# Optimization experiments

Measured on AMD Instinct MI355X. Metric: run time of the kernel, lower is better.

## Reference

```python
import jax, jax.numpy as jnp
import numpy as np

N = 100000   # nodes
E = 3200000  # edges (avg degree 32)
D = 128      # embed_dim
H = 512      # FF hidden
EPS = 1e-5   # BatchNorm eps


def setup_inputs() -> dict:
    key = jax.random.key(0)
    ks = jax.random.split(key, 10)
    x = jax.random.normal(ks[0], (N, D), dtype=jnp.float32)
    edge_index = jax.random.randint(ks[1], (2, E), 0, N, dtype=jnp.int32)
    s = 1.0 / np.sqrt(D)
    W = jax.random.uniform(ks[2], (D, D), jnp.float32, -s, s)   # GCNConv weight
    b = jnp.zeros((D,), jnp.float32)                             # GCNConv bias
    gamma = jnp.ones((D,), jnp.float32)                          # shared BN affine
    beta = jnp.zeros((D,), jnp.float32)
    s1 = 1.0 / np.sqrt(D)
    w1 = jax.random.uniform(ks[3], (D, H), jnp.float32, -s1, s1)
    b1 = jax.random.uniform(ks[4], (H,), jnp.float32, -s1, s1)
    s2 = 1.0 / np.sqrt(H)
    w2 = jax.random.uniform(ks[5], (H, D), jnp.float32, -s2, s2)
    b2 = jax.random.uniform(ks[6], (D,), jnp.float32, -s2, s2)
    return {"x": x, "edge_index": edge_index, "W": W, "b": b,
            "gamma": gamma, "beta": beta, "w1": w1, "b1": b1, "w2": w2, "b2": b2}


def batchnorm(x, gamma, beta):
    # training-mode BatchNorm1d over node dim, biased variance
    mu = jnp.mean(x, axis=0)
    var = jnp.mean(jnp.square(x - mu), axis=0)
    return (x - mu) * jax.lax.rsqrt(var + EPS) * gamma + beta


def gcn_conv(x, edge_index, W, b):
    # PyG GCNConv: add self-loops, sym-normalize, linear, scatter-add, bias
    n = x.shape[0]
    loops = jnp.arange(n, dtype=edge_index.dtype)
    src = jnp.concatenate([edge_index[0], loops])
    dst = jnp.concatenate([edge_index[1], loops])
    xw = x @ W                                                    # [N, D]
    deg = jax.ops.segment_sum(jnp.ones_like(dst, x.dtype), dst, num_segments=n)
    dinv = jax.lax.rsqrt(deg)                                     # deg >= 1 (self-loops)
    norm = dinv[src] * dinv[dst]                                  # [E+N]
    msg = xw[src] * norm[:, None]                                 # [E+N, D] gather
    out = jax.ops.segment_sum(msg, dst, num_segments=n)           # scatter-add
    return out + b


def reference(x, edge_index, W, b, gamma, beta, w1, b1, w2, b2):
    h = gcn_conv(x, edge_index, W, b)
    x = batchnorm(x + h, gamma, beta)
    ff = jax.nn.relu(x @ w1 + b1) @ w2 + b2
    return batchnorm(x + ff, gamma, beta)
```

## Files before the change

### kernel.cpp

```cpp
#include <hip/hip_runtime.h>
#include <hip/hip_bf16.h>
#include <stdint.h>

#define NN 100000
#define NE 3200000
#define DIM 128
#define HID 512
#define BN_EPS 1e-5f
#define NBIN 128
#define NPBIN 784
#define TILE 2048
#define CAP 27000

typedef short short8 __attribute__((ext_vector_type(8)));
typedef float floatx4 __attribute__((ext_vector_type(4)));

__device__ __forceinline__ float bfu2f(unsigned short u) {
    return __uint_as_float(((unsigned int)u) << 16);
}
__device__ __forceinline__ unsigned short f2bfu(float f) {
    union { __hip_bfloat16 h; unsigned short u; } cv;
    cv.h = __float2bfloat16(f);
    return cv.u;
}

__global__ void k_init(int* __restrict__ bincur, float* __restrict__ stats) {
    int i = blockIdx.x * 256 + threadIdx.x;
    if (i < NBIN) bincur[i] = i * CAP;
    if (i < 512) stats[i] = 0.f;
}

__global__ __launch_bounds__(256) void k_fill1(const int* __restrict__ src, const int* __restrict__ dst,
                                               int* __restrict__ bincur, unsigned int* __restrict__ recs) {
    __shared__ int lhist[NBIN], lbase[NBIN], gbase[NBIN];
    __shared__ unsigned int lrec[TILE];
    int tid = threadIdx.x;
    int tbase = blockIdx.x * TILE;
    if (tid < NBIN) lhist[tid] = 0;
    __syncthreads();
    unsigned int myrec[8];
    int mybin[8], myrank[8];
    #pragma unroll
    for (int j = 0; j < 8; ++j) {
        int e = tbase + j * 256 + tid;
        mybin[j] = -1;
        if (e < NE) {
            int d = __builtin_nontemporal_load(dst + e);
            int s = __builtin_nontemporal_load(src + e);
            int b = d / NPBIN;
            myrec[j] = (unsigned)s | ((unsigned)(d - b * NPBIN) << 17);
            mybin[j] = b;
            myrank[j] = atomicAdd(&lhist[b], 1);
        }
    }
    __syncthreads();
    if (tid == 0) {
        int run = 0;
        #pragma unroll
        for (int b = 0; b < NBIN; ++b) { lbase[b] = run; run += lhist[b]; }
    }
    __syncthreads();
    if (tid < NBIN) gbase[tid] = atomicAdd(&bincur[tid], lhist[tid]);
    __syncthreads();
    #pragma unroll
    for (int j = 0; j < 8; ++j)
        if (mybin[j] >= 0) lrec[lbase[mybin[j]] + myrank[j]] = myrec[j];
    __syncthreads();
    int total = lbase[NBIN - 1] + lhist[NBIN - 1];
    for (int i = tid; i < total; i += 256) {
        int b = 0;
        #pragma unroll
        for (int st = NBIN / 2; st > 0; st >>= 1)
            if (b + st < NBIN && lbase[b + st] <= i) b += st;
        int p = gbase[b] + (i - lbase[b]);
        if (p < (b + 1) * CAP) recs[p] = lrec[i];
    }
}

__global__ __launch_bounds__(256) void k_cnt(const unsigned int* __restrict__ recs,
                                             const int* __restrict__ bincur,
                                             int* __restrict__ cnt) {
    __shared__ int lhist[NPBIN];
    int b = blockIdx.x;
    int tid = threadIdx.x;
    for (int i = tid; i < NPBIN; i += 256) lhist[i] = 0;
    __syncthreads();
    int start = b * CAP;
    int end = bincur[b];
    if (end > start + CAP) end = start + CAP;
    if (end < start) end = start;
    for (int i = start + tid; i < end; i += 256) {
        unsigned int r = __builtin_nontemporal_load(recs + i);
        int dl = (int)(r >> 17);
        if (dl < NPBIN) atomicAdd(&lhist[dl], 1);
    }
    __syncthreads();
    for (int i = tid; i < NPBIN; i += 256) {
        int n = b * NPBIN + i;
        if (n < NN) cnt[n] = lhist[i];
    }
}

__global__ __launch_bounds__(1024) void k_scanA(const int* __restrict__ cnt, int* __restrict__ offs,
                                                int* __restrict__ bsum, float* __restrict__ dinv) {
    __shared__ int wsum[16];
    int t = threadIdx.x;
    int lane = t & 63, wid = t >> 6;
    int i = blockIdx.x * 1024 + t;
    int v = (i < NN) ? cnt[i] : 0;
    int incl = v;
    #pragma unroll
    for (int off = 1; off < 64; off <<= 1) {
        int y = __shfl_up(incl, off, 64);
        if (lane >= off) incl += y;
    }
    if (lane == 63) wsum[wid] = incl;
    __syncthreads();
    if (wid == 0) {
        int wv = (lane < 16) ? wsum[lane] : 0;
        int wincl = wv;
        #pragma unroll
        for (int off = 1; off < 16; off <<= 1) {
            int y = __shfl_up(wincl, off, 64);
            if (lane >= off) wincl += y;
        }
        if (lane < 16) wsum[lane] = wincl - wv;
    }
    __syncthreads();
    int excl = wsum[wid] + incl - v;
    if (i < NN) {
        offs[i] = excl;
        dinv[i] = rsqrtf((float)(v + 1));
    }
    if (t == 1023) bsum[blockIdx.x] = excl + v;
}

__global__ __launch_bounds__(128) void k_scanB(int* __restrict__ bsum, int* __restrict__ offs, int nblk) {
    int t = threadIdx.x;
    if (t < 64) {
        int v = (t < nblk) ? bsum[t] : 0;
        int v2 = (t + 64 < nblk) ? bsum[t + 64] : 0;
        int incl = v;
        #pragma unroll
        for (int off = 1; off < 64; off <<= 1) {
            int y = __shfl_up(incl, off, 64);
            if (t >= off) incl += y;
        }
        int tot0 = __shfl(incl, 63, 64);
        int incl2 = v2;
        #pragma unroll
        for (int off = 1; off < 64; off <<= 1) {
            int y = __shfl_up(incl2, off, 64);
            if (t >= off) incl2 += y;
        }
        if (t < nblk) bsum[t] = incl - v;
        if (t + 64 < nblk) bsum[t + 64] = tot0 + incl2 - v2;
        if (t == 63) offs[NN] = tot0 + __shfl(incl2, 63, 64);
    }
}

__global__ void k_scanC(int* __restrict__ offs, const int* __restrict__ bsum) {
    int i = blockIdx.x * 256 + threadIdx.x;
    if (i < NN) offs[i] += bsum[i >> 10];
}

__global__ __launch_bounds__(256) void k_fill2(const unsigned int* __restrict__ recs,
                                               const int* __restrict__ bincur,
                                               const int* __restrict__ offs,
                                               int* __restrict__ srcs) {
    __shared__ int loffs[NPBIN], lcur[NPBIN];
    int b = blockIdx.x;
    int tid = threadIdx.x;
    for (int i = tid; i < NPBIN; i += 256) {
        int n = b * NPBIN + i;
        loffs[i] = (n <= NN) ? offs[n] : NE;
        lcur[i] = 0;
    }
    __syncthreads();
    int start = b * CAP;
    int end = bincur[b];
    if (end > start + CAP) end = start + CAP;
    if (end < start) end = start;
    for (int i = start + tid; i < end; i += 256) {
        unsigned int r = __builtin_nontemporal_load(recs + i);
        int s = (int)(r & 0x1FFFFu);
        int dl = (int)(r >> 17);
        if (dl < NPBIN) {
            int p = loffs[dl] + atomicAdd(&lcur[dl], 1);
            if ((unsigned)p < NE) srcs[p] = s;
        }
    }
}

__global__ void k_wt(const float* __restrict__ W, unsigned short* __restrict__ wt) {
    int i = blockIdx.x * 256 + threadIdx.x;
    if (i < DIM * DIM) {
        int k = i >> 7, n = i & 127;
        wt[n * DIM + k] = f2bfu(W[k * DIM + n]);
    }
}

__global__ void k_prep(const float* __restrict__ w1, const float* __restrict__ w2,
                       unsigned short* __restrict__ w1t, unsigned short* __restrict__ w2t) {
    int i = blockIdx.x * 256 + threadIdx.x;
    if (i < HID * DIM) {
        int n1 = i >> 7, k1 = i & 127;
        w1t[i] = f2bfu(w1[k1 * HID + n1]);
        int n2 = i & 127, k2 = i >> 7;
        w2t[n2 * HID + k2] = f2bfu(w2[k2 * DIM + n2]);
    }
}

__global__ __launch_bounds__(256) void k_gemm1(const float* __restrict__ x,
                                               const unsigned short* __restrict__ wt,
                                               const float* __restrict__ dinv,
                                               unsigned short* __restrict__ xw) {
    int wave = threadIdx.x >> 6;
    int lane = threadIdx.x & 63;
    int row0 = blockIdx.x * 64 + wave * 16;
    int arow = row0 + (lane & 15);
    if (arow >= NN) arow = NN - 1;
    int kbase = (lane >> 4) * 8;
    const float* xr = x + (size_t)arow * DIM;
    short8 afrag[4];
    #pragma unroll
    for (int kt = 0; kt < 4; ++kt) {
        float4 f0 = *(const float4*)(xr + kt * 32 + kbase);
        float4 f1 = *(const float4*)(xr + kt * 32 + kbase + 4);
        short8 a;
        a[0] = (short)f2bfu(f0.x); a[1] = (short)f2bfu(f0.y);
        a[2] = (short)f2bfu(f0.z); a[3] = (short)f2bfu(f0.w);
        a[4] = (short)f2bfu(f1.x); a[5] = (short)f2bfu(f1.y);
        a[6] = (short)f2bfu(f1.z); a[7] = (short)f2bfu(f1.w);
        afrag[kt] = a;
    }
    int crow = row0 + (lane >> 4) * 4;
    float dv[4];
    #pragma unroll
    for (int i = 0; i < 4; ++i) {
        int r = crow + i;
        dv[i] = dinv[r < NN ? r : NN - 1];
    }
    #pragma unroll
    for (int ct = 0; ct < 8; ++ct) {
        int ncol = ct * 16 + (lane & 15);
        const short* wr = (const short*)wt + (size_t)ncol * DIM;
        floatx4 acc = {0.f, 0.f, 0.f, 0.f};
        #pragma unroll
        for (int kt = 0; kt < 4; ++kt) {
            short8 bfrag = *(const short8*)(wr + kt * 32 + kbase);
            acc = __builtin_amdgcn_mfma_f32_16x16x32_bf16(afrag[kt], bfrag, acc, 0, 0, 0);
        }
        #pragma unroll
        for (int i = 0; i < 4; ++i) {
            int r = crow + i;
            if (r < NN) xw[(size_t)r * DIM + ct * 16 + (lane & 15)] = f2bfu(acc[i] * dv[i]);
        }
    }
}

__global__ __launch_bounds__(256) void k_aggregate(const unsigned int* __restrict__ xw2,
                                                   const int* __restrict__ offs,
                                                   const int* __restrict__ srcs,
                                                   const float* __restrict__ dinv,
                                                   const float* __restrict__ x,
                                                   const float* __restrict__ bias,
                                                   unsigned int* __restrict__ u) {
    int node = blockIdx.x * 4 + (threadIdx.x >> 6);
    if (node >= NN) return;
    int lane = threadIdx.x & 63;
    int qt = lane >> 4;
    int ql = lane & 15;
    int beg = offs[node], end = offs[node + 1];
    beg = max(0, min(beg, NE));
    end = max(beg, min(end, NE));
    int ne = end - beg;
    float a[8];
    #pragma unroll
    for (int j = 0; j < 8; ++j) a[j] = 0.f;
    const uint4* xw16 = (const uint4*)xw2;
    for (int base = 0; base < ne; base += 64) {
        int rem = ne - base;
        if (rem > 64) rem = 64;
        int sidx = (lane < rem) ? srcs[beg + base + lane] : 0;
        #pragma unroll 4
        for (int i = 0; i < rem; i += 4) {
            int want = i + qt;
            int s = __builtin_amdgcn_ds_bpermute(want << 2, sidx);
            if (want < rem) {
                if ((unsigned)s >= NN) s = 0;
                uint4 pk = xw16[(size_t)s * 16 + ql];
                a[0] += __uint_as_float(pk.x << 16);
                a[1] += __uint_as_float(pk.x & 0xffff0000u);
                a[2] += __uint_as_float(pk.y << 16);
                a[3] += __uint_as_float(pk.y & 0xffff0000u);
                a[4] += __uint_as_float(pk.z << 16);
                a[5] += __uint_as_float(pk.z & 0xffff0000u);
                a[6] += __uint_as_float(pk.w << 16);
                a[7] += __uint_as_float(pk.w & 0xffff0000u);
            }
        }
    }
    #pragma unroll
    for (int j = 0; j < 8; ++j) {
        a[j] += __shfl_xor(a[j], 16, 64);
        a[j] += __shfl_xor(a[j], 32, 64);
    }
    if (qt == 0) {
        uint4 ps = xw16[(size_t)node * 16 + ql];
        float di = dinv[node];
        const float* xr = x + (size_t)node * DIM + ql * 8;
        float4 xv0 = *(const float4*)xr;
        float4 xv1 = *(const float4*)(xr + 4);
        float4 bv0 = *(const float4*)(bias + ql * 8);
        float4 bv1 = *(const float4*)(bias + ql * 8 + 4);
        float o0 = xv0.x + bv0.x + di * (a[0] + __uint_as_float(ps.x << 16));
        float o1 = xv0.y + bv0.y + di * (a[1] + __uint_as_float(ps.x & 0xffff0000u));
        float o2 = xv0.z + bv0.z + di * (a[2] + __uint_as_float(ps.y << 16));
        float o3 = xv0.w + bv0.w + di * (a[3] + __uint_as_float(ps.y & 0xffff0000u));
        float o4 = xv1.x + bv1.x + di * (a[4] + __uint_as_float(ps.z << 16));
        float o5 = xv1.y + bv1.y + di * (a[5] + __uint_as_float(ps.z & 0xffff0000u));
        float o6 = xv1.z + bv1.z + di * (a[6] + __uint_as_float(ps.w << 16));
        float o7 = xv1.w + bv1.w + di * (a[7] + __uint_as_float(ps.w & 0xffff0000u));
        uint4 pk;
        pk.x = ((unsigned int)f2bfu(o1) << 16) | (unsigned int)f2bfu(o0);
        pk.y = ((unsigned int)f2bfu(o3) << 16) | (unsigned int)f2bfu(o2);
        pk.z = ((unsigned int)f2bfu(o5) << 16) | (unsigned int)f2bfu(o4);
        pk.w = ((unsigned int)f2bfu(o7) << 16) | (unsigned int)f2bfu(o6);
        ((uint4*)u)[(size_t)node * 16 + ql] = pk;
    }
}

__global__ void k_stats(const unsigned int* __restrict__ u2, float* __restrict__ stats) {
    int t = threadIdx.x;
    int c = t & 63, g = t >> 6;
    float s0 = 0.f, q0 = 0.f, s1 = 0.f, q1 = 0.f;
    for (int r = blockIdx.x * 4 + g; r < NN; r += gridDim.x * 4) {
        unsigned int pv = u2[(size_t)r * 64 + c];
        float x0 = __uint_as_float(pv << 16);
        float x1 = __uint_as_float(pv & 0xffff0000u);
        s0 += x0; q0 += x0 * x0; s1 += x1; q1 += x1 * x1;
    }
    __shared__ float A[256], B[256], C[256], D2[256];
    A[t] = s0; B[t] = q0; C[t] = s1; D2[t] = q1;
    __syncthreads();
    if (t < 64) {
        float rs0 = A[t] + A[t + 64] + A[t + 128] + A[t + 192];
        float rq0 = B[t] + B[t + 64] + B[t + 128] + B[t + 192];
        float rs1 = C[t] + C[t + 64] + C[t + 128] + C[t + 192];
        float rq1 = D2[t] + D2[t + 64] + D2[t + 128] + D2[t + 192];
        atomicAdd(&stats[2 * c],           rs0);
        atomicAdd(&stats[2 * c + 1],       rs1);
        atomicAdd(&stats[DIM + 2 * c],     rq0);
        atomicAdd(&stats[DIM + 2 * c + 1], rq1);
    }
}

__global__ void k_stats2(const float2* __restrict__ v2, float* __restrict__ stats) {
    int t = threadIdx.x;
    int c = t & 63, g = t >> 6;
    float s0 = 0.f, q0 = 0.f, s1 = 0.f, q1 = 0.f;
    for (int r = blockIdx.x * 4 + g; r < NN; r += gridDim.x * 4) {
        float2 pv = v2[(size_t)r * 64 + c];
        s0 += pv.x; q0 += pv.x * pv.x; s1 += pv.y; q1 += pv.y * pv.y;
    }
    __shared__ float A[256], B[256], C[256], D2[256];
    A[t] = s0; B[t] = q0; C[t] = s1; D2[t] = q1;
    __syncthreads();
    if (t < 64) {
        float rs0 = A[t] + A[t + 64] + A[t + 128] + A[t + 192];
        float rq0 = B[t] + B[t + 64] + B[t + 128] + B[t + 192];
        float rs1 = C[t] + C[t + 64] + C[t + 128] + C[t + 192];
        float rq1 = D2[t] + D2[t + 64] + D2[t + 128] + D2[t + 192];
        atomicAdd(&stats[2 * c],           rs0);
        atomicAdd(&stats[2 * c + 1],       rs1);
        atomicAdd(&stats[DIM + 2 * c],     rq0);
        atomicAdd(&stats[DIM + 2 * c + 1], rq1);
    }
}

__global__ __launch_bounds__(512) void k_ffx(const unsigned int* __restrict__ u2,
                                             const float* __restrict__ stats1,
                                             const float* __restrict__ gamma,
                                             const float* __restrict__ beta,
                                             const unsigned short* __restrict__ w1t,
                                             const float* __restrict__ b1,
                                             const unsigned short* __restrict__ w2t,
                                             const float* __restrict__ b2,
                                             float* __restrict__ v) {
    __shared__ __align__(16) float sscale[DIM], sshift[DIM];
    __shared__ __align__(16) unsigned int sw1[64 * 64];
    __shared__ __align__(16) unsigned int sw2[128 * 32];
    __shared__ __align__(16) unsigned int hbufs[8][16 * 32];
    int tid = threadIdx.x;
    if (tid < DIM) {
        float mu  = stats1[tid] * (1.0f / NN);
        float var = stats1[DIM + tid] * (1.0f / NN) - mu * mu;
        float sc = rsqrtf(var + BN_EPS) * gamma[tid];
        sscale[tid] = sc;
        sshift[tid] = beta[tid] - mu * sc;
    }
    __syncthreads();
    int wave = tid >> 6, lane = tid & 63;
    int m = lane & 15, q = lane >> 4;
    int nb = blockIdx.x * 256 + wave * 32;
    unsigned int* hb = &hbufs[wave][0];
    const int xsw = (m & 7) * 4;

    short8 yfrag[2][4];
    #pragma unroll
    for (int s = 0; s < 2; ++s) {
        int ng = nb + s * 16 + m;
        if (ng >= NN) ng = NN - 1;
        const uint4* up = (const uint4*)(u2 + (size_t)ng * 64);
        #pragma unroll
        for (int kt = 0; kt < 4; ++kt) {
            uint4 pv = up[kt * 4 + q];
            int c0 = kt * 32 + q * 8;
            float4 sa = *(const float4*)&sscale[c0], sb = *(const float4*)&sscale[c0 + 4];
            float4 ha = *(const float4*)&sshift[c0], hbv = *(const float4*)&sshift[c0 + 4];
            float f0 = __uint_as_float(pv.x << 16)         * sa.x + ha.x;
            float f1 = __uint_as_float(pv.x & 0xffff0000u) * sa.y + ha.y;
            float f2 = __uint_as_float(pv.y << 16)         * sa.z + ha.z;
            float f3 = __uint_as_float(pv.y & 0xffff0000u) * sa.w + ha.w;
            float f4 = __uint_as_float(pv.z << 16)         * sb.x + hbv.x;
            float f5 = __uint_as_float(pv.z & 0xffff0000u) * sb.y + hbv.y;
            float f6 = __uint_as_float(pv.w << 16)         * sb.z + hbv.z;
            float f7 = __uint_as_float(pv.w & 0xffff0000u) * sb.w + hbv.w;
            union { unsigned int u[4]; short8 sv; } yf;
            yf.u[0] = ((unsigned int)f2bfu(f1) << 16) | f2bfu(f0);
            yf.u[1] = ((unsigned int)f2bfu(f3) << 16) | f2bfu(f2);
            yf.u[2] = ((unsigned int)f2bfu(f5) << 16) | f2bfu(f4);
            yf.u[3] = ((unsigned int)f2bfu(f7) << 16) | f2bfu(f6);
            yfrag[s][kt] = yf.sv;
        }
    }

    floatx4 acc2[2][8];
    #pragma unroll
    for (int s = 0; s < 2; ++s)
        #pragma unroll
        for (int t = 0; t < 8; ++t) acc2[s][t] = (floatx4){0.f, 0.f, 0.f, 0.f};

    const uint4* w1g = (const uint4*)w1t;
    const uint4* w2g = (const uint4*)w2t;

    for (int c = 0; c < 8; ++c) {
        __syncthreads();
        #pragma unroll
        for (int it = 0; it < 2; ++it) {
            int i = tid + it * 512;
            int j = i >> 4, s4 = i & 15;
            uint4 val = w1g[(size_t)(c * 64 + j) * 16 + s4];
            *(uint4*)&sw1[j * 64 + ((s4 * 4) ^ ((j & 7) * 4))] = val;
        }
        #pragma unroll
        for (int it = 0; it < 2; ++it) {
            int i = tid + it * 512;
            int n = i >> 3, s4 = i & 7;
            uint4 val = w2g[(size_t)n * 64 + c * 8 + s4];
            *(uint4*)&sw2[n * 32 + ((s4 * 4) ^ ((n & 7) * 4))] = val;
        }
        __syncthreads();
        #pragma unroll
        for (int s = 0; s < 2; ++s) {
            floatx4 acc1[4];
            #pragma unroll
            for (int t = 0; t < 4; ++t) acc1[t] = (floatx4){0.f, 0.f, 0.f, 0.f};
            #pragma unroll
            for (int kt = 0; kt < 4; ++kt) {
                #pragma unroll
                for (int t = 0; t < 4; ++t) {
                    short8 wf = *(const short8*)&sw1[(t * 16 + m) * 64 + ((kt * 16 + q * 4) ^ xsw)];
                    acc1[t] = __builtin_amdgcn_mfma_f32_16x16x32_bf16(wf, yfrag[s][kt], acc1[t], 0, 0, 0);
                }
            }
            #pragma unroll
            for (int t = 0; t < 4; ++t) {
                float4 bb = *(const float4*)&b1[c * 64 + t * 16 + q * 4];
                float h0 = fmaxf(acc1[t][0] + bb.x, 0.f);
                float h1 = fmaxf(acc1[t][1] + bb.y, 0.f);
                float h2 = fmaxf(acc1[t][2] + bb.z, 0.f);
                float h3 = fmaxf(acc1[t][3] + bb.w, 0.f);
                uint2 hp;
                hp.x = ((unsigned int)f2bfu(h1) << 16) | f2bfu(h0);
                hp.y = ((unsigned int)f2bfu(h3) << 16) | f2bfu(h2);
                *(uint2*)&hb[m * 32 + ((t * 8 + q * 2) ^ xsw)] = hp;
            }
            #pragma unroll
            for (int kt = 0; kt < 2; ++kt) {
                short8 hf = *(const short8*)&hb[m * 32 + ((kt * 16 + q * 4) ^ xsw)];
                #pragma unroll
                for (int t = 0; t < 8; ++t) {
                    short8 wf2 = *(const short8*)&sw2[(t * 16 + m) * 32 + ((kt * 16 + q * 4) ^ xsw)];
                    acc2[s][t] = __builtin_amdgcn_mfma_f32_16x16x32_bf16(hf, wf2, acc2[s][t], 0, 0, 0);
                }
            }
        }
    }
    #pragma unroll
    for (int s = 0; s < 2; ++s) {
        #pragma unroll
        for (int t = 0; t < 8; ++t) {
            int col = t * 16 + m;
            float b2v = b2[col];
            float scl = sscale[col], shf = sshift[col];
            #pragma unroll
            for (int i = 0; i < 4; ++i) {
                int ng = nb + s * 16 + q * 4 + i;
                if (ng < NN) {
                    unsigned int pv = u2[(size_t)ng * 64 + (col >> 1)];
                    float uval = (col & 1) ? __uint_as_float(pv & 0xffff0000u)
                                           : __uint_as_float(pv << 16);
                    v[(size_t)ng * DIM + col] = acc2[s][t][i] + b2v + (uval * scl + shf);
                }
            }
        }
    }
}

__global__ void k_final(float* buf, const float* __restrict__ stats2,
                        const float* __restrict__ gamma,
                        const float* __restrict__ beta) {
    __shared__ float ssc[DIM], ssh[DIM];
    int t = threadIdx.x;
    if (t < DIM) {
        float mu  = stats2[t] * (1.0f / NN);
        float var = stats2[DIM + t] * (1.0f / NN) - mu * mu;
        float rsg = rsqrtf(var + BN_EPS) * gamma[t];
        ssc[t] = rsg;
        ssh[t] = beta[t] - mu * rsg;
    }
    __syncthreads();
    const int total = NN * DIM / 4;
    float4* b4 = (float4*)buf;
    for (int i = blockIdx.x * blockDim.x + t; i < total; i += gridDim.x * blockDim.x) {
        float4 val = b4[i];
        int c = (i * 4) & (DIM - 1);
        val.x = val.x * ssc[c]     + ssh[c];
        val.y = val.y * ssc[c + 1] + ssh[c + 1];
        val.z = val.z * ssc[c + 2] + ssh[c + 2];
        val.w = val.w * ssc[c + 3] + ssh[c + 3];
        b4[i] = val;
    }
}

extern "C" void kernel_launch(void* const* d_in, const int* in_sizes, int n_in,
                              void* d_out, int out_size, void* d_ws, size_t ws_size,
                              hipStream_t stream) {
    const float* x     = (const float*)d_in[0];
    const int*   ei    = (const int*)d_in[1];
    const float* W     = (const float*)d_in[2];
    const float* b     = (const float*)d_in[3];
    const float* gamma = (const float*)d_in[4];
    const float* beta  = (const float*)d_in[5];
    const float* w1    = (const float*)d_in[6];
    const float* b1    = (const float*)d_in[7];
    const float* w2    = (const float*)d_in[8];
    const float* b2    = (const float*)d_in[9];

    char* p = (char*)d_ws;
    auto alloc = [&](size_t bytes) { char* r = p; p += (bytes + 255) & ~(size_t)255; return r; };
    unsigned int*   u     = (unsigned int*)alloc((size_t)NN * DIM * 2);
    int*            cnt   = (int*)alloc((size_t)NN * 4);
    int*            offs  = (int*)alloc((size_t)(NN + 1) * 4);
    float*          dinv  = (float*)alloc((size_t)NN * 4);
    int*            bsum  = (int*)alloc(128 * 4);
    int*            bincur = (int*)alloc((size_t)NBIN * 4);
    unsigned short* wt    = (unsigned short*)alloc((size_t)DIM * DIM * 2);
    unsigned short* w1t   = (unsigned short*)alloc((size_t)HID * DIM * 2);
    unsigned short* w2t   = (unsigned short*)alloc((size_t)HID * DIM * 2);
    float*          stats = (float*)alloc(512 * 4);

    unsigned short* xw   = (unsigned short*)d_out;
    unsigned int*   recs = (unsigned int*)d_out;
    int*            srcs = (int*)((char*)d_out + (size_t)NN * DIM * 2);
    float*          v    = (float*)d_out;

    const int* esrc = ei;
    const int* edst = ei + NE;
    const int nblk = (NN + 1023) / 1024;
    const int n1blk = (NE + TILE - 1) / TILE;

    k_init<<<2, 256, 0, stream>>>(bincur, stats);
    k_fill1<<<n1blk, 256, 0, stream>>>(esrc, edst, bincur, recs);
    k_cnt<<<NBIN, 256, 0, stream>>>(recs, bincur, cnt);
    k_scanA<<<nblk, 1024, 0, stream>>>(cnt, offs, bsum, dinv);
    k_scanB<<<1, 128, 0, stream>>>(bsum, offs, nblk);
    k_scanC<<<(NN + 255) / 256, 256, 0, stream>>>(offs, bsum);
    k_fill2<<<NBIN, 256, 0, stream>>>(recs, bincur, offs, srcs);
    k_wt<<<(DIM * DIM + 255) / 256, 256, 0, stream>>>(W, wt);
    k_prep<<<(HID * DIM + 255) / 256, 256, 0, stream>>>(w1, w2, w1t, w2t);
    k_gemm1<<<(NN + 63) / 64, 256, 0, stream>>>(x, wt, dinv, xw);
    k_aggregate<<<(NN + 3) / 4, 256, 0, stream>>>((const unsigned int*)xw, offs, srcs, dinv, x, b, u);
    k_stats<<<512, 256, 0, stream>>>(u, stats);
    k_ffx<<<(NN + 255) / 256, 512, 0, stream>>>(u, stats, gamma, beta, w1t, b1, w2t, b2, v);
    k_stats2<<<512, 256, 0, stream>>>((const float2*)v, stats + 256);
    k_final<<<2048, 256, 0, stream>>>((float*)d_out, stats + 256, gamma, beta);
}
```

Measured before the change: 589.0 us.

## Double-buffer FFN weight tiles in LDS via async global-to-LDS loads

```diff
diff --git a/kernel.cpp b/kernel.cpp
--- a/kernel.cpp
+++ b/kernel.cpp
@@ -12,6 +12,13 @@
 #define TILE 2048
 #define CAP 27000
 
+#define SW1_OFF 0
+#define SW2_OFF 8192
+#define HB_OFF  16384
+#define SC_OFF  20480
+#define SH_OFF  20608
+#define FFX_LDS_BYTES (20736 * 4)
+
 typedef short short8 __attribute__((ext_vector_type(8)));
 typedef float floatx4 __attribute__((ext_vector_type(4)));
 
@@ -22,6 +29,12 @@
     union { __hip_bfloat16 h; unsigned short u; } cv;
     cv.h = __float2bfloat16(f);
     return cv.u;
+}
+
+__device__ __forceinline__ void gld16(const unsigned int* g, unsigned int* l) {
+    __builtin_amdgcn_global_load_lds(
+        (const __attribute__((address_space(1))) unsigned int*)g,
+        (__attribute__((address_space(3))) unsigned int*)l, 16, 0, 0);
 }
 
 __global__ void k_init(int* __restrict__ bincur, float* __restrict__ stats) {
@@ -388,10 +401,9 @@
                                              const unsigned short* __restrict__ w2t,
                                              const float* __restrict__ b2,
                                              float* __restrict__ v) {
-    __shared__ __align__(16) float sscale[DIM], sshift[DIM];
-    __shared__ __align__(16) unsigned int sw1[64 * 64];
-    __shared__ __align__(16) unsigned int sw2[128 * 32];
-    __shared__ __align__(16) unsigned int hbufs[8][16 * 32];
+    extern __shared__ unsigned int smem[];
+    float* sscale = (float*)(smem + SC_OFF);
+    float* sshift = (float*)(smem + SH_OFF);
     int tid = threadIdx.x;
     if (tid < DIM) {
         float mu  = stats1[tid] * (1.0f / NN);
@@ -404,8 +416,25 @@
     int wave = tid >> 6, lane = tid & 63;
     int m = lane & 15, q = lane >> 4;
     int nb = blockIdx.x * 256 + wave * 32;
-    unsigned int* hb = &hbufs[wave][0];
+    unsigned int* hb = smem + HB_OFF + wave * 512;
     const int xsw = (m & 7) * 4;
+
+    const uint4* w1g = (const uint4*)w1t;
+    const uint4* w2g = (const uint4*)w2t;
+
+    auto stage = [&](int c, int buf) {
+        #pragma unroll
+        for (int it = 0; it < 2; ++it) {
+            int i = tid + it * 512;
+            int j = i >> 4, s4 = i & 15;
+            gld16((const unsigned int*)&w1g[(size_t)(c * 64 + j) * 16 + (s4 ^ (j & 7))],
+                  smem + SW1_OFF + buf * 4096 + i * 4);
+            int n = i >> 3, s8 = i & 7;
+            gld16((const unsigned int*)&w2g[(size_t)n * 64 + c * 8 + (s8 ^ (n & 7))],
+                  smem + SW2_OFF + buf * 4096 + i * 4);
+        }
+    };
+    stage(0, 0);
 
     short8 yfrag[2][4];
     #pragma unroll
@@ -442,26 +471,12 @@
         #pragma unroll
         for (int t = 0; t < 8; ++t) acc2[s][t] = (floatx4){0.f, 0.f, 0.f, 0.f};
 
-    const uint4* w1g = (const uint4*)w1t;
-    const uint4* w2g = (const uint4*)w2t;
-
     for (int c = 0; c < 8; ++c) {
+        int cur = c & 1;
         __syncthreads();
-        #pragma unroll
-        for (int it = 0; it < 2; ++it) {
-            int i = tid + it * 512;
-            int j = i >> 4, s4 = i & 15;
-            uint4 val = w1g[(size_t)(c * 64 + j) * 16 + s4];
-            *(uint4*)&sw1[j * 64 + ((s4 * 4) ^ ((j & 7) * 4))] = val;
-        }
-        #pragma unroll
-        for (int it = 0; it < 2; ++it) {
-            int i = tid + it * 512;
-            int n = i >> 3, s4 = i & 7;
-            uint4 val = w2g[(size_t)n * 64 + c * 8 + s4];
-            *(uint4*)&sw2[n * 32 + ((s4 * 4) ^ ((n & 7) * 4))] = val;
-        }
-        __syncthreads();
+        if (c < 7) stage(c + 1, cur ^ 1);
+        const unsigned int* sw1 = smem + SW1_OFF + cur * 4096;
+        const unsigned int* sw2 = smem + SW2_OFF + cur * 4096;
         #pragma unroll
         for (int s = 0; s < 2; ++s) {
             floatx4 acc1[4];
@@ -594,7 +609,7 @@
     k_gemm1<<<(NN + 63) / 64, 256, 0, stream>>>(x, wt, dinv, xw);
     k_aggregate<<<(NN + 3) / 4, 256, 0, stream>>>((const unsigned int*)xw, offs, srcs, dinv, x, b, u);
     k_stats<<<512, 256, 0, stream>>>(u, stats);
-    k_ffx<<<(NN + 255) / 256, 512, 0, stream>>>(u, stats, gamma, beta, w1t, b1, w2t, b2, v);
+    k_ffx<<<(NN + 255) / 256, 512, FFX_LDS_BYTES, stream>>>(u, stats, gamma, beta, w1t, b1, w2t, b2, v);
     k_stats2<<<512, 256, 0, stream>>>((const float2*)v, stats + 256);
     k_final<<<2048, 256, 0, stream>>>((float*)d_out, stats + 256, gamma, beta);
 }
```

Result: faster. 556.5 us (-5.5%).
